# Optimization experiments

Measured on AMD Instinct MI355X. Metric: run time of the kernel, lower is better.

Reference implementation:

```python
import jax, jax.numpy as jnp
import numpy as np

N_NODES = 100000
N_EDGES = 1600000


def gcn_conv(x, row, col, norm, W, b, n_nodes):
    # PyG GCNConv: h = x @ W; aggregate normalized messages over (A + I); add bias
    h = x @ W                                   # [N, out]
    msg = h[col] * norm[:, None]                # [E+N, out] gather + scale
    out = jax.ops.segment_sum(msg, row, num_segments=n_nodes)  # scatter-add
    return out + b


def _norm_and_loops(edge_index, n_nodes):
    # add self-loops, compute symmetric normalization coefficients
    row = jnp.concatenate([edge_index[0], jnp.arange(n_nodes, dtype=edge_index.dtype)])
    col = jnp.concatenate([edge_index[1], jnp.arange(n_nodes, dtype=edge_index.dtype)])
    deg = jax.ops.segment_sum(jnp.ones_like(row, dtype=jnp.float32), row,
                              num_segments=n_nodes)
    dinv = jnp.where(deg > 0, jax.lax.rsqrt(deg), 0.0)
    norm = dinv[row] * dinv[col]
    return row, col, norm


def reference(x, edge_index, W1, b1, W2, b2, W3, b3):
    n_nodes = x.shape[0]
    row, col, norm = _norm_and_loops(edge_index, n_nodes)
    h = jax.nn.relu(gcn_conv(x, row, col, norm, W1, b1, n_nodes))
    h = jax.nn.relu(gcn_conv(h, row, col, norm, W2, b2, n_nodes))
    h = gcn_conv(h, row, col, norm, W3, b3, n_nodes)
    return jax.nn.log_softmax(h, axis=1)


def setup_inputs() -> dict:
    key = jax.random.key(0)
    ks = jax.random.split(key, 5)
    d_in, d_hid, d_out = 128, 128, 16
    x = jax.random.normal(ks[0], (N_NODES, d_in), dtype=jnp.float32)
    edge_index = jax.random.randint(ks[1], (2, N_EDGES), 0, N_NODES, dtype=jnp.int64)
    s1 = 1.0 / np.sqrt(d_in)
    s3 = 1.0 / np.sqrt(d_hid)
    W1 = jax.random.normal(ks[2], (d_in, d_hid), dtype=jnp.float32) * s1
    W2 = jax.random.normal(ks[3], (d_hid, d_hid), dtype=jnp.float32) * s3
    W3 = jax.random.normal(ks[4], (d_hid, d_out), dtype=jnp.float32) * s3
    return {
        "x": x, "edge_index": edge_index,
        "W1": W1, "b1": jnp.zeros((d_hid,), jnp.float32),
        "W2": W2, "b2": jnp.zeros((d_hid,), jnp.float32),
        "W3": W3, "b3": jnp.zeros((d_out,), jnp.float32),
    }
```

## Files before the change

### kernel.cpp

```cpp
#include <hip/hip_runtime.h>

typedef unsigned int u32;
typedef _Float16 f16;
typedef __attribute__((ext_vector_type(8))) _Float16 half8;
typedef __attribute__((ext_vector_type(2))) _Float16 half2_t;
typedef __attribute__((ext_vector_type(4))) float f32x4;

#define D_IN 128
#define D_HID 128
#define D_OUT 16
#define RPB 128
#define MAXBUCK 1024
#define CHUNK 10240
#define PGRAN 4
#define CAP 3072
#define PCAP 3584


__device__ inline int load_row(const int* ei, u32 f, int e, int E) {
    return f ? ei[e] : ei[2 * e];
}
__device__ inline int load_col(const int* ei, u32 f, int e, int E) {
    return f ? ei[E + e] : ei[2 * E + 2 * e];
}
__device__ inline int clampi(int v, int n) {
    v = v < 0 ? 0 : v;
    return v >= n ? n - 1 : v;
}

__global__ __launch_bounds__(256) void scatter_k(const int* __restrict__ ei,
                                                 u32* __restrict__ bcnt,
                                                 u32* __restrict__ bdata,
                                                 int E, int N, int NBK) {
    __shared__ u32 lcnt[MAXBUCK];
    __shared__ u32 lflag;
    int tid = threadIdx.x;
    if (tid == 0) lflag = 0;
    for (int i = tid; i < NBK; i += 256) lcnt[i] = 0;
    __syncthreads();
    int nw = (2 * E < 8192) ? 2 * E : 8192;
    for (int k = tid * 2 + 1; k < nw; k += 512)
        if (ei[k] != 0) atomicOr(&lflag, 1u);
    __syncthreads();
    u32 f = lflag;
    int base = blockIdx.x * CHUNK;
    int lim = base + CHUNK < E ? base + CHUNK : E;
    for (int e = base + tid; e < lim; e += 1024) {
        int e1 = e + 256, e2 = e + 512, e3 = e + 768;
        int r0 = clampi(load_row(ei, f, e, E), N);
        int r1 = (e1 < lim) ? clampi(load_row(ei, f, e1, E), N) : -1;
        int r2 = (e2 < lim) ? clampi(load_row(ei, f, e2, E), N) : -1;
        int r3 = (e3 < lim) ? clampi(load_row(ei, f, e3, E), N) : -1;
        atomicAdd(&lcnt[(u32)r0 >> 7], 1u);
        if (r1 >= 0) atomicAdd(&lcnt[(u32)r1 >> 7], 1u);
        if (r2 >= 0) atomicAdd(&lcnt[(u32)r2 >> 7], 1u);
        if (r3 >= 0) atomicAdd(&lcnt[(u32)r3 >> 7], 1u);
    }
    __syncthreads();
    for (int i = tid; i < NBK; i += 256) {
        u32 c = lcnt[i];
        lcnt[i] = c ? atomicAdd(&bcnt[i], c) : 0u;
    }
    __syncthreads();
    for (int e = base + tid; e < lim; e += 1024) {
        int e1 = e + 256, e2 = e + 512, e3 = e + 768;
        int r0 = clampi(load_row(ei, f, e, E), N);
        int c0 = clampi(load_col(ei, f, e, E), N);
        int r1 = -1, c1 = 0, r2 = -1, c2 = 0, r3 = -1, c3 = 0;
        if (e1 < lim) { r1 = clampi(load_row(ei, f, e1, E), N); c1 = clampi(load_col(ei, f, e1, E), N); }
        if (e2 < lim) { r2 = clampi(load_row(ei, f, e2, E), N); c2 = clampi(load_col(ei, f, e2, E), N); }
        if (e3 < lim) { r3 = clampi(load_row(ei, f, e3, E), N); c3 = clampi(load_col(ei, f, e3, E), N); }
        u32 b0 = (u32)r0 >> 7;
        u32 pos = atomicAdd(&lcnt[b0], 1u);
        if (pos < CAP) bdata[(size_t)b0 * CAP + pos] = ((u32)(r0 & (RPB - 1)) << 20) | (u32)c0;
        if (r1 >= 0) {
            u32 b = (u32)r1 >> 7;
            pos = atomicAdd(&lcnt[b], 1u);
            if (pos < CAP) bdata[(size_t)b * CAP + pos] = ((u32)(r1 & (RPB - 1)) << 20) | (u32)c1;
        }
        if (r2 >= 0) {
            u32 b = (u32)r2 >> 7;
            pos = atomicAdd(&lcnt[b], 1u);
            if (pos < CAP) bdata[(size_t)b * CAP + pos] = ((u32)(r2 & (RPB - 1)) << 20) | (u32)c2;
        }
        if (r3 >= 0) {
            u32 b = (u32)r3 >> 7;
            pos = atomicAdd(&lcnt[b], 1u);
            if (pos < CAP) bdata[(size_t)b * CAP + pos] = ((u32)(r3 & (RPB - 1)) << 20) | (u32)c3;
        }
    }
}

__global__ __launch_bounds__(256) void finalize_k(const u32* __restrict__ bdata,
                                                  const u32* __restrict__ bcnt,
                                                  uint2* __restrict__ rdesc,
                                                  float* __restrict__ dinv,
                                                  u32* __restrict__ ecol,
                                                  int N) {
    __shared__ u32 smc[RPB];
    __shared__ u32 cur[RPB];
    int b = blockIdx.x;
    int tid = threadIdx.x;
    u32 cnt = bcnt[b];
    if (cnt > CAP) cnt = CAP;
    u32 s = (u32)b * CAP;
    u32 t = s + cnt;
    u32 pbase = (u32)b * PCAP;
    if (tid < RPB) smc[tid] = 0;
    __syncthreads();
    for (u32 i = s + tid; i < t; i += 256)
        atomicAdd(&smc[bdata[i] >> 20], 1u);
    __syncthreads();
    u32 deg = (tid < RPB) ? smc[tid] : 0;
    u32 pdeg = (deg + PGRAN - 1) & ~(u32)(PGRAN - 1);
    if (tid < RPB) smc[tid] = pdeg;
    __syncthreads();
    for (int off = 1; off < RPB; off <<= 1) {
        u32 tv = (tid < RPB && tid >= off) ? smc[tid - off] : 0u;
        __syncthreads();
        if (tid < RPB) smc[tid] += tv;
        __syncthreads();
    }
    u32 pexcl = (tid < RPB) ? (smc[tid] - pdeg) : 0;
    if (tid < RPB) {
        int r = b * RPB + tid;
        if (r < N) {
            rdesc[r] = make_uint2(pbase + pexcl, pbase + pexcl + pdeg);
            dinv[r] = rsqrtf((float)(deg + 1u));
        }
        cur[tid] = pbase + pexcl;
    }
    __syncthreads();
    for (u32 i = s + tid; i < t; i += 256) {
        u32 rec = bdata[i];
        u32 pos = atomicAdd(&cur[rec >> 20], 1u);
        ecol[pos] = rec & 0xFFFFFu;
    }
    __syncthreads();
    if (tid < RPB) {
        u32 st = pbase + pexcl;
        for (u32 k = deg; k < pdeg; k++) ecol[st + k] = (u32)N;
    }
}

__global__ __launch_bounds__(256) void reformat_all(const float* __restrict__ W1,
                                                    const float* __restrict__ W2,
                                                    const float* __restrict__ W3,
                                                    f16* __restrict__ W1h, f16* __restrict__ W1l,
                                                    f16* __restrict__ W2h, f16* __restrict__ W2l,
                                                    f16* __restrict__ W3h, f16* __restrict__ W3l,
                                                    f16* __restrict__ hzero,
                                                    f16* __restrict__ h3zero) {
    if (blockIdx.x == 17) {
        int tix = threadIdx.x;
        if (tix < 128) hzero[tix] = (f16)0;
        else if (tix < 144) h3zero[tix - 128] = (f16)0;
        return;
    }
    const float* W;
    f16 *Wh, *Wl;
    int ntiles, bidx;
    if (blockIdx.x < 8) { W = W1; Wh = W1h; Wl = W1l; ntiles = 8; bidx = blockIdx.x; }
    else if (blockIdx.x < 16) { W = W2; Wh = W2h; Wl = W2l; ntiles = 8; bidx = blockIdx.x - 8; }
    else { W = W3; Wh = W3h; Wl = W3l; ntiles = 1; bidx = 0; }
    int idx = bidx * 256 + threadIdx.x;
    int total = 4 * ntiles * 64;
    if (idx >= total) return;
    int lane = idx & 63;
    int st = idx >> 6;
    int t = st % ntiles;
    int s = st / ntiles;
    int Nc = ntiles * 16;
    int n = t * 16 + (lane & 15);
    int kb = lane >> 4;
    half8 vh, vl;
#pragma unroll
    for (int j = 0; j < 8; j++) {
        float w = W[(size_t)(s * 32 + kb * 8 + j) * Nc + n];
        f16 hi = (f16)w;
        f16 lo = (f16)(w - (float)hi);
        vh[j] = hi;
        vl[j] = lo;
    }
    *(half8*)(Wh + (size_t)idx * 8) = vh;
    *(half8*)(Wl + (size_t)idx * 8) = vl;
}


__global__ __launch_bounds__(256) void gemm128_l1(const float* __restrict__ A,
                                                  const f16* __restrict__ Wh,
                                                  const f16* __restrict__ Wl,
                                                  const float* __restrict__ dinv,
                                                  f16* __restrict__ H, int M) {
    __shared__ f16 sBh[2048 * 8];
    __shared__ f16 sBl[2048 * 8];
    for (int i = threadIdx.x; i < 2048; i += 256) {
        *(half8*)(sBh + (size_t)i * 8) = *(const half8*)(Wh + (size_t)i * 8);
        *(half8*)(sBl + (size_t)i * 8) = *(const half8*)(Wl + (size_t)i * 8);
    }
    int wave = threadIdx.x >> 6, lane = threadIdx.x & 63;
    int mbase = blockIdx.x * 64 + wave * 16;
    int mload = mbase + (lane & 15);
    if (mload >= M) mload = M - 1;
    int kq = lane >> 4;
    f32x4 a0[4], a1[4];
#pragma unroll
    for (int s = 0; s < 4; s++) {
        const float* ap = A + (size_t)mload * 128 + s * 32 + kq * 8;
        a0[s] = *(const f32x4*)ap;
        a1[s] = *(const f32x4*)(ap + 4);
    }
    f32x4 acc[8];
#pragma unroll
    for (int t = 0; t < 8; t++) acc[t] = (f32x4){0.f, 0.f, 0.f, 0.f};
    __syncthreads();
#pragma unroll
    for (int s = 0; s < 4; s++) {
        half8 ah, al;
#pragma unroll
        for (int j = 0; j < 4; j++) {
            float v = a0[s][j];
            f16 hi = (f16)v;
            ah[j] = hi;
            al[j] = (f16)(v - (float)hi);
            float w = a1[s][j];
            f16 wi = (f16)w;
            ah[j + 4] = wi;
            al[j + 4] = (f16)(w - (float)wi);
        }
#pragma unroll
        for (int t = 0; t < 8; t++) {
            half8 bh = *(const half8*)(sBh + (size_t)((s * 8 + t) * 64 + lane) * 8);
            half8 bl = *(const half8*)(sBl + (size_t)((s * 8 + t) * 64 + lane) * 8);
            acc[t] = __builtin_amdgcn_mfma_f32_16x16x32_f16(ah, bh, acc[t], 0, 0, 0);
            acc[t] = __builtin_amdgcn_mfma_f32_16x16x32_f16(ah, bl, acc[t], 0, 0, 0);
            acc[t] = __builtin_amdgcn_mfma_f32_16x16x32_f16(al, bh, acc[t], 0, 0, 0);
        }
    }
    int coln = lane & 15;
    int rbase = mbase + ((lane >> 4) << 2);
    float dsc[4];
#pragma unroll
    for (int i = 0; i < 4; i++) {
        int rr = rbase + i;
        dsc[i] = dinv[rr < M ? rr : M - 1];
    }
#pragma unroll
    for (int t = 0; t < 8; t++) {
#pragma unroll
        for (int i = 0; i < 4; i++) {
            int rr = rbase + i;
            if (rr < M) H[(size_t)rr * 128 + t * 16 + coln] = (f16)(acc[t][i] * dsc[i]);
        }
    }
}

__global__ __launch_bounds__(256) void gemm128_l2(const f16* __restrict__ A,
                                                  const f16* __restrict__ Wh,
                                                  const f16* __restrict__ Wl,
                                                  f16* __restrict__ H, int M) {
    __shared__ f16 sBh[2048 * 8];
    __shared__ f16 sBl[2048 * 8];
    for (int i = threadIdx.x; i < 2048; i += 256) {
        *(half8*)(sBh + (size_t)i * 8) = *(const half8*)(Wh + (size_t)i * 8);
        *(half8*)(sBl + (size_t)i * 8) = *(const half8*)(Wl + (size_t)i * 8);
    }
    int wave = threadIdx.x >> 6, lane = threadIdx.x & 63;
    int mbase = blockIdx.x * 64 + wave * 16;
    int mload = mbase + (lane & 15);
    if (mload >= M) mload = M - 1;
    int kq = lane >> 4;
    half8 a[4];
#pragma unroll
    for (int s = 0; s < 4; s++)
        a[s] = *(const half8*)(A + (size_t)mload * 128 + s * 32 + kq * 8);
    f32x4 acc[8];
#pragma unroll
    for (int t = 0; t < 8; t++) acc[t] = (f32x4){0.f, 0.f, 0.f, 0.f};
    __syncthreads();
#pragma unroll
    for (int s = 0; s < 4; s++) {
#pragma unroll
        for (int t = 0; t < 8; t++) {
            half8 bh = *(const half8*)(sBh + (size_t)((s * 8 + t) * 64 + lane) * 8);
            half8 bl = *(const half8*)(sBl + (size_t)((s * 8 + t) * 64 + lane) * 8);
            acc[t] = __builtin_amdgcn_mfma_f32_16x16x32_f16(a[s], bh, acc[t], 0, 0, 0);
            acc[t] = __builtin_amdgcn_mfma_f32_16x16x32_f16(a[s], bl, acc[t], 0, 0, 0);
        }
    }
    int coln = lane & 15;
    int rbase = mbase + ((lane >> 4) << 2);
#pragma unroll
    for (int t = 0; t < 8; t++) {
#pragma unroll
        for (int i = 0; i < 4; i++) {
            int rr = rbase + i;
            if (rr < M) H[(size_t)rr * 128 + t * 16 + coln] = (f16)acc[t][i];
        }
    }
}

__global__ __launch_bounds__(256) void gemm16(const f16* __restrict__ A,
                                              const f16* __restrict__ Wh,
                                              const f16* __restrict__ Wl,
                                              f16* __restrict__ H, int M) {
    __shared__ f16 sBh[256 * 8];
    __shared__ f16 sBl[256 * 8];
    if (threadIdx.x < 256) {
        int i = threadIdx.x;
        *(half8*)(sBh + (size_t)i * 8) = *(const half8*)(Wh + (size_t)i * 8);
        *(half8*)(sBl + (size_t)i * 8) = *(const half8*)(Wl + (size_t)i * 8);
    }
    int wave = threadIdx.x >> 6, lane = threadIdx.x & 63;
    int mbase = blockIdx.x * 64 + wave * 16;
    int mload = mbase + (lane & 15);
    if (mload >= M) mload = M - 1;
    int kq = lane >> 4;
    half8 a[4];
#pragma unroll
    for (int s = 0; s < 4; s++)
        a[s] = *(const half8*)(A + (size_t)mload * 128 + s * 32 + kq * 8);
    f32x4 acc = (f32x4){0.f, 0.f, 0.f, 0.f};
    __syncthreads();
#pragma unroll
    for (int s = 0; s < 4; s++) {
        half8 bh = *(const half8*)(sBh + (size_t)(s * 64 + lane) * 8);
        half8 bl = *(const half8*)(sBl + (size_t)(s * 64 + lane) * 8);
        acc = __builtin_amdgcn_mfma_f32_16x16x32_f16(a[s], bh, acc, 0, 0, 0);
        acc = __builtin_amdgcn_mfma_f32_16x16x32_f16(a[s], bl, acc, 0, 0, 0);
    }
    int coln = lane & 15;
    int rbase = mbase + ((lane >> 4) << 2);
#pragma unroll
    for (int i = 0; i < 4; i++) {
        int rr = rbase + i;
        if (rr < M) H[(size_t)rr * 16 + coln] = (f16)acc[i];
    }
}

__global__ __launch_bounds__(256) void agg128(const f16* __restrict__ h,
                                              const u32* __restrict__ ecol,
                                              const uint2* __restrict__ rdesc,
                                              const float* __restrict__ dinv,
                                              const float* __restrict__ bias,
                                              f16* __restrict__ out, int M) {
    int lane = threadIdx.x & 63;
    int wave = __builtin_amdgcn_readfirstlane(threadIdx.x >> 6);
    int r = blockIdx.x * 4 + wave;
    if (r >= M) return;
    uint2 d = rdesc[r];
    u32 e = (u32)__builtin_amdgcn_readfirstlane((int)d.x);
    u32 end = (u32)__builtin_amdgcn_readfirstlane((int)d.y);
    float dr = dinv[r];
    const char* hb = (const char*)h;
    u32 loff = (u32)lane << 2;
    float2 bb = ((const float2*)bias)[lane];
    half2_t vs = *(const half2_t*)(hb + (((u32)r << 8) + loff));
    float ax0 = 0, ay0 = 0, ax1 = 0, ay1 = 0, ax2 = 0, ay2 = 0, ax3 = 0, ay3 = 0;
    for (; e + 16 <= end; e += 16) {
        const u32* ep = ecol + e;
        u32 c[16];
#pragma unroll
        for (int j = 0; j < 16; j++) c[j] = ep[j];
        half2_t v[16];
#pragma unroll
        for (int j = 0; j < 16; j++)
            v[j] = *(const half2_t*)(hb + ((c[j] << 8) + loff));
#pragma unroll
        for (int j = 0; j < 16; j += 4) {
            ax0 = fmaf((float)v[j][0],     dr, ax0); ay0 = fmaf((float)v[j][1],     dr, ay0);
            ax1 = fmaf((float)v[j + 1][0], dr, ax1); ay1 = fmaf((float)v[j + 1][1], dr, ay1);
            ax2 = fmaf((float)v[j + 2][0], dr, ax2); ay2 = fmaf((float)v[j + 2][1], dr, ay2);
            ax3 = fmaf((float)v[j + 3][0], dr, ax3); ay3 = fmaf((float)v[j + 3][1], dr, ay3);
        }
    }
    for (; e < end; e += 4) {
        const u32* ep = ecol + e;
        u32 c0 = ep[0], c1 = ep[1], c2 = ep[2], c3 = ep[3];
        half2_t v0 = *(const half2_t*)(hb + ((c0 << 8) + loff));
        half2_t v1 = *(const half2_t*)(hb + ((c1 << 8) + loff));
        half2_t v2 = *(const half2_t*)(hb + ((c2 << 8) + loff));
        half2_t v3 = *(const half2_t*)(hb + ((c3 << 8) + loff));
        ax0 = fmaf((float)v0[0], dr, ax0); ay0 = fmaf((float)v0[1], dr, ay0);
        ax1 = fmaf((float)v1[0], dr, ax1); ay1 = fmaf((float)v1[1], dr, ay1);
        ax2 = fmaf((float)v2[0], dr, ax2); ay2 = fmaf((float)v2[1], dr, ay2);
        ax3 = fmaf((float)v3[0], dr, ax3); ay3 = fmaf((float)v3[1], dr, ay3);
    }
    float ax = ((ax0 + ax1) + (ax2 + ax3)) + fmaf((float)vs[0], dr, bb.x);
    float ay = ((ay0 + ay1) + (ay2 + ay3)) + fmaf((float)vs[1], dr, bb.y);
    ax = fmaxf(ax, 0.f) * dr;
    ay = fmaxf(ay, 0.f) * dr;
    half2_t o;
    o[0] = (f16)ax;
    o[1] = (f16)ay;
    ((half2_t*)out)[(size_t)r * 64 + lane] = o;
}

__global__ __launch_bounds__(256) void agg16_lsm(const f16* __restrict__ h3,
                                                 const u32* __restrict__ ecol,
                                                 const uint2* __restrict__ rdesc,
                                                 const float* __restrict__ dinv,
                                                 const float* __restrict__ bias,
                                                 float* __restrict__ out, int M) {
    int g = threadIdx.x >> 4, l = threadIdx.x & 15;
    int r = blockIdx.x * 16 + g;
    if (r >= M) return;
    uint2 d = rdesc[r];
    u32 beg = d.x, end = d.y;
    float dr = dinv[r];
    float bl = bias[l];
    float self = (float)h3[(size_t)r * 16 + l];
    float a0 = 0.f, a1 = 0.f, a2 = 0.f, a3 = 0.f;
    u32 e = beg;
    for (; e + 8 <= end; e += 8) {
        u32 c[8];
#pragma unroll
        for (int j = 0; j < 8; j++) c[j] = ecol[e + j];
        f16 v[8];
#pragma unroll
        for (int j = 0; j < 8; j++) v[j] = h3[(size_t)c[j] * 16 + l];
        a0 += (float)v[0] + (float)v[4];
        a1 += (float)v[1] + (float)v[5];
        a2 += (float)v[2] + (float)v[6];
        a3 += (float)v[3] + (float)v[7];
    }
    if (e < end) {
        u32 c[4];
#pragma unroll
        for (int j = 0; j < 4; j++) c[j] = ecol[e + j];
        f16 v[4];
#pragma unroll
        for (int j = 0; j < 4; j++) v[j] = h3[(size_t)c[j] * 16 + l];
        a0 += (float)v[0];
        a1 += (float)v[1];
        a2 += (float)v[2];
        a3 += (float)v[3];
    }
    float acc = (((a0 + a1) + (a2 + a3)) + self) * dr + bl;
    float m = acc;
#pragma unroll
    for (int o = 8; o >= 1; o >>= 1) m = fmaxf(m, __shfl_xor(m, o, 16));
    float ex = expf(acc - m);
    float s = ex;
#pragma unroll
    for (int o = 8; o >= 1; o >>= 1) s += __shfl_xor(s, o, 16);
    out[(size_t)r * 16 + l] = acc - m - logf(s);
}


extern "C" void kernel_launch(void* const* d_in, const int* in_sizes, int n_in,
                              void* d_out, int out_size, void* d_ws, size_t ws_size,
                              hipStream_t stream) {
    const float* x = (const float*)d_in[0];
    const int* ei = (const int*)d_in[1];
    const float* W1 = (const float*)d_in[2];
    const float* b1 = (const float*)d_in[3];
    const float* W2 = (const float*)d_in[4];
    const float* b2 = (const float*)d_in[5];
    const float* W3 = (const float*)d_in[6];
    const float* b3 = (const float*)d_in[7];
    int N = in_sizes[0] / D_IN;
    int E = in_sizes[1] / 2;

    int NBK = (N + RPB - 1) / RPB;
    int NB = (E + CHUNK - 1) / CHUNK;

    char* p = (char*)d_ws;
    auto alloc = [&](size_t bytes) -> void* {
        void* q = (void*)p;
        p += (bytes + 255) & ~(size_t)255;
        return q;
    };
    u32* bcnt = (u32*)alloc((size_t)NBK * 4);
    float* dinv = (float*)alloc((size_t)N * 4);
    uint2* rdesc = (uint2*)alloc((size_t)(N + 1) * 8);
    u32* bdata = (u32*)alloc((size_t)NBK * CAP * 4);
    u32* ecol = (u32*)alloc((size_t)NBK * PCAP * 4 + 256);
    f16* wf1h = (f16*)alloc(16384 * 2);
    f16* wf1l = (f16*)alloc(16384 * 2);
    f16* wf2h = (f16*)alloc(16384 * 2);
    f16* wf2l = (f16*)alloc(16384 * 2);
    f16* wf3h = (f16*)alloc(2048 * 2);
    f16* wf3l = (f16*)alloc(2048 * 2);
    f16* h = (f16*)alloc((size_t)(N + 1) * 128 * 2);
    f16* act = (f16*)alloc((size_t)N * 128 * 2);
    f16* h3 = (f16*)alloc((size_t)(N + 1) * 16 * 2);
    (void)ws_size; (void)n_in; (void)out_size;

    hipMemsetAsync(bcnt, 0, (size_t)NBK * 4, stream);

    scatter_k<<<NB, 256, 0, stream>>>(ei, bcnt, bdata, E, N, NBK);
    finalize_k<<<NBK, 256, 0, stream>>>(bdata, bcnt, rdesc, dinv, ecol, N);

    reformat_all<<<18, 256, 0, stream>>>(W1, W2, W3, wf1h, wf1l, wf2h, wf2l,
                                         wf3h, wf3l,
                                         h + (size_t)N * 128,
                                         h3 + (size_t)N * 16);

    int gb = (N + 63) / 64;
    int ab = (N + 3) / 4;
    gemm128_l1<<<gb, 256, 0, stream>>>(x, wf1h, wf1l, dinv, h, N);
    agg128<<<ab, 256, 0, stream>>>(h, ecol, rdesc, dinv, b1, act, N);
    gemm128_l2<<<gb, 256, 0, stream>>>(act, wf2h, wf2l, h, N);
    agg128<<<ab, 256, 0, stream>>>(h, ecol, rdesc, dinv, b2, act, N);
    gemm16<<<gb, 256, 0, stream>>>(act, wf3h, wf3l, h3, N);
    agg16_lsm<<<(N + 15) / 16, 256, 0, stream>>>(h3, ecol, rdesc,
                                                 dinv, b3, (float*)d_out, N);
}
```

Measured before the change: 334.3 us.

## Fold weight reformat into scatter kernel and double GEMM rows per block

The weight split/reformat work moves into extra blocks appended to the scatter kernel, which removes one kernel launch. The two 128-wide GEMMs now process 128 rows per block, two 16-row tiles per wave, instead of 64. This halves how often each block reloads the weights into shared memory and gives each B fragment read from LDS twice as many MFMAs. The cost is higher register pressure from the doubled accumulators and A fragments, which may reduce occupancy.

```diff
diff --git a/kernel.cpp b/kernel.cpp
--- a/kernel.cpp
+++ b/kernel.cpp
@@ -31,7 +31,52 @@
 __global__ __launch_bounds__(256) void scatter_k(const int* __restrict__ ei,
                                                  u32* __restrict__ bcnt,
                                                  u32* __restrict__ bdata,
-                                                 int E, int N, int NBK) {
+                                                 int E, int N, int NBK, int NB,
+                                                 const float* __restrict__ W1,
+                                                 const float* __restrict__ W2,
+                                                 const float* __restrict__ W3,
+                                                 f16* __restrict__ W1h, f16* __restrict__ W1l,
+                                                 f16* __restrict__ W2h, f16* __restrict__ W2l,
+                                                 f16* __restrict__ W3h, f16* __restrict__ W3l,
+                                                 f16* __restrict__ hzero,
+                                                 f16* __restrict__ h3zero) {
+    if (blockIdx.x >= (u32)NB) {
+        int rb = blockIdx.x - NB;
+        if (rb == 17) {
+            int tix = threadIdx.x;
+            if (tix < 128) hzero[tix] = (f16)0;
+            else if (tix < 144) h3zero[tix - 128] = (f16)0;
+            return;
+        }
+        const float* W;
+        f16 *Wh, *Wl;
+        int ntiles, bidx;
+        if (rb < 8) { W = W1; Wh = W1h; Wl = W1l; ntiles = 8; bidx = rb; }
+        else if (rb < 16) { W = W2; Wh = W2h; Wl = W2l; ntiles = 8; bidx = rb - 8; }
+        else { W = W3; Wh = W3h; Wl = W3l; ntiles = 1; bidx = 0; }
+        int idx = bidx * 256 + threadIdx.x;
+        int total = 4 * ntiles * 64;
+        if (idx >= total) return;
+        int lane = idx & 63;
+        int st = idx >> 6;
+        int t = st % ntiles;
+        int s = st / ntiles;
+        int Nc = ntiles * 16;
+        int n = t * 16 + (lane & 15);
+        int kb = lane >> 4;
+        half8 vh, vl;
+#pragma unroll
+        for (int j = 0; j < 8; j++) {
+            float w = W[(size_t)(s * 32 + kb * 8 + j) * Nc + n];
+            f16 hi = (f16)w;
+            f16 lo = (f16)(w - (float)hi);
+            vh[j] = hi;
+            vl[j] = lo;
+        }
+        *(half8*)(Wh + (size_t)idx * 8) = vh;
+        *(half8*)(Wl + (size_t)idx * 8) = vl;
+        return;
+    }
     __shared__ u32 lcnt[MAXBUCK];
     __shared__ u32 lflag;
     int tid = threadIdx.x;
@@ -143,49 +188,6 @@
     }
 }
 
-__global__ __launch_bounds__(256) void reformat_all(const float* __restrict__ W1,
-                                                    const float* __restrict__ W2,
-                                                    const float* __restrict__ W3,
-                                                    f16* __restrict__ W1h, f16* __restrict__ W1l,
-                                                    f16* __restrict__ W2h, f16* __restrict__ W2l,
-                                                    f16* __restrict__ W3h, f16* __restrict__ W3l,
-                                                    f16* __restrict__ hzero,
-                                                    f16* __restrict__ h3zero) {
-    if (blockIdx.x == 17) {
-        int tix = threadIdx.x;
-        if (tix < 128) hzero[tix] = (f16)0;
-        else if (tix < 144) h3zero[tix - 128] = (f16)0;
-        return;
-    }
-    const float* W;
-    f16 *Wh, *Wl;
-    int ntiles, bidx;
-    if (blockIdx.x < 8) { W = W1; Wh = W1h; Wl = W1l; ntiles = 8; bidx = blockIdx.x; }
-    else if (blockIdx.x < 16) { W = W2; Wh = W2h; Wl = W2l; ntiles = 8; bidx = blockIdx.x - 8; }
-    else { W = W3; Wh = W3h; Wl = W3l; ntiles = 1; bidx = 0; }
-    int idx = bidx * 256 + threadIdx.x;
-    int total = 4 * ntiles * 64;
-    if (idx >= total) return;
-    int lane = idx & 63;
-    int st = idx >> 6;
-    int t = st % ntiles;
-    int s = st / ntiles;
-    int Nc = ntiles * 16;
-    int n = t * 16 + (lane & 15);
-    int kb = lane >> 4;
-    half8 vh, vl;
-#pragma unroll
-    for (int j = 0; j < 8; j++) {
-        float w = W[(size_t)(s * 32 + kb * 8 + j) * Nc + n];
-        f16 hi = (f16)w;
-        f16 lo = (f16)(w - (float)hi);
-        vh[j] = hi;
-        vl[j] = lo;
-    }
-    *(half8*)(Wh + (size_t)idx * 8) = vh;
-    *(half8*)(Wl + (size_t)idx * 8) = vl;
-}
-
 
 __global__ __launch_bounds__(256) void gemm128_l1(const float* __restrict__ A,
                                                   const f16* __restrict__ Wh,
@@ -199,58 +201,75 @@
         *(half8*)(sBl + (size_t)i * 8) = *(const half8*)(Wl + (size_t)i * 8);
     }
     int wave = threadIdx.x >> 6, lane = threadIdx.x & 63;
-    int mbase = blockIdx.x * 64 + wave * 16;
-    int mload = mbase + (lane & 15);
-    if (mload >= M) mload = M - 1;
     int kq = lane >> 4;
-    f32x4 a0[4], a1[4];
+    int mb[2], ml[2];
+    mb[0] = blockIdx.x * 128 + wave * 16;
+    mb[1] = mb[0] + 64;
+#pragma unroll
+    for (int t2 = 0; t2 < 2; t2++) {
+        ml[t2] = mb[t2] + (lane & 15);
+        if (ml[t2] >= M) ml[t2] = M - 1;
+    }
+    f32x4 a0[2][4], a1[2][4];
+#pragma unroll
+    for (int t2 = 0; t2 < 2; t2++)
+#pragma unroll
+        for (int s = 0; s < 4; s++) {
+            const float* ap = A + (size_t)ml[t2] * 128 + s * 32 + kq * 8;
+            a0[t2][s] = *(const f32x4*)ap;
+            a1[t2][s] = *(const f32x4*)(ap + 4);
+        }
+    f32x4 acc[2][8];
+#pragma unroll
+    for (int t2 = 0; t2 < 2; t2++)
+#pragma unroll
+        for (int t = 0; t < 8; t++) acc[t2][t] = (f32x4){0.f, 0.f, 0.f, 0.f};
+    __syncthreads();
 #pragma unroll
     for (int s = 0; s < 4; s++) {
-        const float* ap = A + (size_t)mload * 128 + s * 32 + kq * 8;
-        a0[s] = *(const f32x4*)ap;
-        a1[s] = *(const f32x4*)(ap + 4);
-    }
-    f32x4 acc[8];
-#pragma unroll
-    for (int t = 0; t < 8; t++) acc[t] = (f32x4){0.f, 0.f, 0.f, 0.f};
-    __syncthreads();
-#pragma unroll
-    for (int s = 0; s < 4; s++) {
-        half8 ah, al;
-#pragma unroll
-        for (int j = 0; j < 4; j++) {
-            float v = a0[s][j];
-            f16 hi = (f16)v;
-            ah[j] = hi;
-            al[j] = (f16)(v - (float)hi);
-            float w = a1[s][j];
-            f16 wi = (f16)w;
-            ah[j + 4] = wi;
-            al[j + 4] = (f16)(w - (float)wi);
-        }
+        half8 ah[2], al[2];
+#pragma unroll
+        for (int t2 = 0; t2 < 2; t2++)
+#pragma unroll
+            for (int j = 0; j < 4; j++) {
+                float v = a0[t2][s][j];
+                f16 hi = (f16)v;
+                ah[t2][j] = hi;
+                al[t2][j] = (f16)(v - (float)hi);
+                float w = a1[t2][s][j];
+                f16 wi = (f16)w;
+                ah[t2][j + 4] = wi;
+                al[t2][j + 4] = (f16)(w - (float)wi);
+            }
 #pragma unroll
         for (int t = 0; t < 8; t++) {
             half8 bh = *(const half8*)(sBh + (size_t)((s * 8 + t) * 64 + lane) * 8);
             half8 bl = *(const half8*)(sBl + (size_t)((s * 8 + t) * 64 + lane) * 8);
-            acc[t] = __builtin_amdgcn_mfma_f32_16x16x32_f16(ah, bh, acc[t], 0, 0, 0);
-            acc[t] = __builtin_amdgcn_mfma_f32_16x16x32_f16(ah, bl, acc[t], 0, 0, 0);
-            acc[t] = __builtin_amdgcn_mfma_f32_16x16x32_f16(al, bh, acc[t], 0, 0, 0);
+            acc[0][t] = __builtin_amdgcn_mfma_f32_16x16x32_f16(ah[0], bh, acc[0][t], 0, 0, 0);
+            acc[0][t] = __builtin_amdgcn_mfma_f32_16x16x32_f16(ah[0], bl, acc[0][t], 0, 0, 0);
+            acc[0][t] = __builtin_amdgcn_mfma_f32_16x16x32_f16(al[0], bh, acc[0][t], 0, 0, 0);
+            acc[1][t] = __builtin_amdgcn_mfma_f32_16x16x32_f16(ah[1], bh, acc[1][t], 0, 0, 0);
+            acc[1][t] = __builtin_amdgcn_mfma_f32_16x16x32_f16(ah[1], bl, acc[1][t], 0, 0, 0);
+            acc[1][t] = __builtin_amdgcn_mfma_f32_16x16x32_f16(al[1], bh, acc[1][t], 0, 0, 0);
         }
     }
     int coln = lane & 15;
-    int rbase = mbase + ((lane >> 4) << 2);
-    float dsc[4];
-#pragma unroll
-    for (int i = 0; i < 4; i++) {
-        int rr = rbase + i;
-        dsc[i] = dinv[rr < M ? rr : M - 1];
-    }
-#pragma unroll
-    for (int t = 0; t < 8; t++) {
+#pragma unroll
+    for (int t2 = 0; t2 < 2; t2++) {
+        int rbase = mb[t2] + ((lane >> 4) << 2);
+        float dsc[4];
 #pragma unroll
         for (int i = 0; i < 4; i++) {
             int rr = rbase + i;
-            if (rr < M) H[(size_t)rr * 128 + t * 16 + coln] = (f16)(acc[t][i] * dsc[i]);
+            dsc[i] = dinv[rr < M ? rr : M - 1];
+        }
+#pragma unroll
+        for (int t = 0; t < 8; t++) {
+#pragma unroll
+            for (int i = 0; i < 4; i++) {
+                int rr = rbase + i;
+                if (rr < M) H[(size_t)rr * 128 + t * 16 + coln] = (f16)(acc[t2][t][i] * dsc[i]);
+            }
         }
     }
 }
@@ -266,17 +285,26 @@
         *(half8*)(sBl + (size_t)i * 8) = *(const half8*)(Wl + (size_t)i * 8);
     }
     int wave = threadIdx.x >> 6, lane = threadIdx.x & 63;
-    int mbase = blockIdx.x * 64 + wave * 16;
-    int mload = mbase + (lane & 15);
-    if (mload >= M) mload = M - 1;
     int kq = lane >> 4;
-    half8 a[4];
-#pragma unroll
-    for (int s = 0; s < 4; s++)
-        a[s] = *(const half8*)(A + (size_t)mload * 128 + s * 32 + kq * 8);
-    f32x4 acc[8];
-#pragma unroll
-    for (int t = 0; t < 8; t++) acc[t] = (f32x4){0.f, 0.f, 0.f, 0.f};
+    int mb[2], ml[2];
+    mb[0] = blockIdx.x * 128 + wave * 16;
+    mb[1] = mb[0] + 64;
+#pragma unroll
+    for (int t2 = 0; t2 < 2; t2++) {
+        ml[t2] = mb[t2] + (lane & 15);
+        if (ml[t2] >= M) ml[t2] = M - 1;
+    }
+    half8 a[2][4];
+#pragma unroll
+    for (int t2 = 0; t2 < 2; t2++)
+#pragma unroll
+        for (int s = 0; s < 4; s++)
+            a[t2][s] = *(const half8*)(A + (size_t)ml[t2] * 128 + s * 32 + kq * 8);
+    f32x4 acc[2][8];
+#pragma unroll
+    for (int t2 = 0; t2 < 2; t2++)
+#pragma unroll
+        for (int t = 0; t < 8; t++) acc[t2][t] = (f32x4){0.f, 0.f, 0.f, 0.f};
     __syncthreads();
 #pragma unroll
     for (int s = 0; s < 4; s++) {
@@ -284,18 +312,23 @@
         for (int t = 0; t < 8; t++) {
             half8 bh = *(const half8*)(sBh + (size_t)((s * 8 + t) * 64 + lane) * 8);
             half8 bl = *(const half8*)(sBl + (size_t)((s * 8 + t) * 64 + lane) * 8);
-            acc[t] = __builtin_amdgcn_mfma_f32_16x16x32_f16(a[s], bh, acc[t], 0, 0, 0);
-            acc[t] = __builtin_amdgcn_mfma_f32_16x16x32_f16(a[s], bl, acc[t], 0, 0, 0);
+            acc[0][t] = __builtin_amdgcn_mfma_f32_16x16x32_f16(a[0][s], bh, acc[0][t], 0, 0, 0);
+            acc[0][t] = __builtin_amdgcn_mfma_f32_16x16x32_f16(a[0][s], bl, acc[0][t], 0, 0, 0);
+            acc[1][t] = __builtin_amdgcn_mfma_f32_16x16x32_f16(a[1][s], bh, acc[1][t], 0, 0, 0);
+            acc[1][t] = __builtin_amdgcn_mfma_f32_16x16x32_f16(a[1][s], bl, acc[1][t], 0, 0, 0);
         }
     }
     int coln = lane & 15;
-    int rbase = mbase + ((lane >> 4) << 2);
-#pragma unroll
-    for (int t = 0; t < 8; t++) {
-#pragma unroll
-        for (int i = 0; i < 4; i++) {
-            int rr = rbase + i;
-            if (rr < M) H[(size_t)rr * 128 + t * 16 + coln] = (f16)acc[t][i];
+#pragma unroll
+    for (int t2 = 0; t2 < 2; t2++) {
+        int rbase = mb[t2] + ((lane >> 4) << 2);
+#pragma unroll
+        for (int t = 0; t < 8; t++) {
+#pragma unroll
+            for (int i = 0; i < 4; i++) {
+                int rr = rbase + i;
+                if (rr < M) H[(size_t)rr * 128 + t * 16 + coln] = (f16)acc[t2][t][i];
+            }
         }
     }
 }
@@ -489,21 +522,21 @@
 
     hipMemsetAsync(bcnt, 0, (size_t)NBK * 4, stream);
 
-    scatter_k<<<NB, 256, 0, stream>>>(ei, bcnt, bdata, E, N, NBK);
+    scatter_k<<<NB + 18, 256, 0, stream>>>(ei, bcnt, bdata, E, N, NBK, NB,
+                                           W1, W2, W3, wf1h, wf1l, wf2h, wf2l,
+                                           wf3h, wf3l,
+                                           h + (size_t)N * 128,
+                                           h3 + (size_t)N * 16);
     finalize_k<<<NBK, 256, 0, stream>>>(bdata, bcnt, rdesc, dinv, ecol, N);
 
-    reformat_all<<<18, 256, 0, stream>>>(W1, W2, W3, wf1h, wf1l, wf2h, wf2l,
-                                         wf3h, wf3l,
-                                         h + (size_t)N * 128,
-                                         h3 + (size_t)N * 16);
-
-    int gb = (N + 63) / 64;
+    int gb128 = (N + 127) / 128;
+    int gb64 = (N + 63) / 64;
     int ab = (N + 3) / 4;
-    gemm128_l1<<<gb, 256, 0, stream>>>(x, wf1h, wf1l, dinv, h, N);
+    gemm128_l1<<<gb128, 256, 0, stream>>>(x, wf1h, wf1l, dinv, h, N);
     agg128<<<ab, 256, 0, stream>>>(h, ecol, rdesc, dinv, b1, act, N);
-    gemm128_l2<<<gb, 256, 0, stream>>>(act, wf2h, wf2l, h, N);
+    gemm128_l2<<<gb128, 256, 0, stream>>>(act, wf2h, wf2l, h, N);
     agg128<<<ab, 256, 0, stream>>>(h, ecol, rdesc, dinv, b2, act, N);
-    gemm16<<<gb, 256, 0, stream>>>(act, wf3h, wf3l, h3, N);
+    gemm16<<<gb64, 256, 0, stream>>>(act, wf3h, wf3l, h3, N);
     agg16_lsm<<<(N + 15) / 16, 256, 0, stream>>>(h3, ecol, rdesc,
                                                  dinv, b3, (float*)d_out, N);
 }
```

New measurement: 332.8 us. Within noise of the previous version (-0.4%).
